# Kernel optimization log

Measured on AMD Instinct MI355X. Metric: run time of the kernel, lower is better.

Reference implementation:

```python
import jax, jax.numpy as jnp
import numpy as np

B_, H_, W_ = 4, 64, 64
D_MODEL, D_INNER, N_STATE, R_RANK, K_ = 96, 192, 16, 6, 4
EPS = 1e-5

def silu(v):
    return v * jax.nn.sigmoid(v)

def setup_inputs() -> dict:
    key = jax.random.key(0)
    ks = jax.random.split(key, 8)
    d, dm = D_INNER, D_MODEL
    A = jnp.tile(jnp.arange(1, N_STATE + 1, dtype=jnp.float32)[None, :], (K_ * d, 1))
    return {
        "x": jax.random.normal(ks[0], (B_, H_, W_, dm), jnp.float32),
        "in_proj_w": jax.random.normal(ks[1], (2 * d, dm), jnp.float32) * 0.02,
        "conv_w": jax.random.normal(ks[2], (d, 1, 3, 3), jnp.float32) * 0.1,
        "conv_b": jnp.zeros((d,), jnp.float32),
        "x_proj_weight": jax.random.normal(ks[3], (K_, R_RANK + 2 * N_STATE, d), jnp.float32) * 0.05,
        "dt_projs_weight": jax.random.normal(ks[4], (K_, d, R_RANK), jnp.float32) * 0.1,
        "dt_projs_bias": jax.random.normal(ks[5], (K_, d), jnp.float32) * 0.1,
        "A_logs": jnp.log(A),
        "Ds": jnp.ones((K_ * d,), jnp.float32),
        "out_norm_w": jnp.ones((d,), jnp.float32),
        "out_norm_b": jnp.zeros((d,), jnp.float32),
        "out_proj_w": jax.random.normal(ks[6], (dm, d), jnp.float32) * 0.02,
    }

def selective_scan(u, dts, As, Bs, Cs, Ds, dt_bias):
    # u, dts: [B,K,D,L]; As: [K,D,N]; Bs, Cs: [B,K,N,L]; Ds, dt_bias: [K,D]
    delta = jax.nn.softplus(dts + dt_bias[None, :, :, None])
    dT = jnp.moveaxis(delta, -1, 0)  # [L,B,K,D]
    uT = jnp.moveaxis(u, -1, 0)      # [L,B,K,D]
    BT = jnp.moveaxis(Bs, -1, 0)     # [L,B,K,N]
    CT = jnp.moveaxis(Cs, -1, 0)     # [L,B,K,N]
    h0 = jnp.zeros((u.shape[0], K_, D_INNER, N_STATE), jnp.float32)

    def step(h, inps):
        dt, ut, bt, ct = inps
        h = jnp.exp(dt[..., None] * As[None]) * h + (dt * ut)[..., None] * bt[:, :, None, :]
        y = jnp.einsum('bkdn,bkn->bkd', h, ct)
        return h, y

    _, ys = jax.lax.scan(step, h0, (dT, uT, BT, CT))
    ys = jnp.moveaxis(ys, 0, -1)  # [B,K,D,L]
    return ys + u * Ds[None, :, :, None]

def reference(x, in_proj_w, conv_w, conv_b, x_proj_weight, dt_projs_weight,
              dt_projs_bias, A_logs, Ds, out_norm_w, out_norm_b, out_proj_w):
    B, H, W, dm = x.shape
    d, N, R, K = D_INNER, N_STATE, R_RANK, K_
    L = H * W
    # in_proj + z gate (SiLU)
    xz = jnp.einsum('bhwc,pc->bhwp', x, in_proj_w)  # [B,H,W,2d]
    xc, z = xz[..., :d], xz[..., d:]
    z = silu(z)
    # depthwise conv (NCHW) + SiLU
    xc = jnp.transpose(xc, (0, 3, 1, 2))  # [B,d,H,W]
    xc = jax.lax.conv_general_dilated(
        xc, conv_w, (1, 1), 'SAME', feature_group_count=d,
        dimension_numbers=('NCHW', 'OIHW', 'NCHW')) + conv_b[None, :, None, None]
    xc = silu(xc)
    # cross-scan: 4 directions
    x0 = xc.reshape(B, d, L)                                   # row-major
    x1 = jnp.transpose(xc, (0, 1, 3, 2)).reshape(B, d, L)       # col-major
    xs = jnp.stack([x0, x1, x0[..., ::-1], x1[..., ::-1]], axis=1)  # [B,K,D,L]
    # projections
    x_dbl = jnp.einsum('bkdl,kcd->bkcl', xs, x_proj_weight)
    dts, Bs, Cs = jnp.split(x_dbl, [R, R + N], axis=2)
    dts = jnp.einsum('bkrl,kdr->bkdl', dts, dt_projs_weight)
    As = -jnp.exp(A_logs).reshape(K, d, N)
    ys = selective_scan(xs, dts, As, Bs, Cs, Ds.reshape(K, d), dt_projs_bias)
    # cross-merge
    y_wh = (ys[:, 1] + ys[:, 3, :, ::-1]).reshape(B, d, W, H)
    y_wh = jnp.transpose(y_wh, (0, 1, 3, 2)).reshape(B, d, L)
    y = ys[:, 0] + ys[:, 2, :, ::-1] + y_wh                     # [B,d,L]
    y = jnp.transpose(y.reshape(B, d, H, W), (0, 2, 3, 1))       # [B,H,W,d]
    # out_norm: LayerNorm over channel dim
    mu = jnp.mean(y, axis=-1, keepdims=True)
    var = jnp.mean((y - mu) ** 2, axis=-1, keepdims=True)
    y = out_norm_w * (y - mu) * jax.lax.rsqrt(var + EPS) + out_norm_b
    # gate + out_proj
    y = y * z
    return jnp.einsum('bhwd,cd->bhwc', y, out_proj_w)
```

## Files before the change

### kernel.cpp

```cpp
#include <hip/hip_runtime.h>
#include <math.h>

#define B_ 4
#define HH 64
#define WW 64
#define LL 4096
#define DM 96
#define DI 192
#define NS 16
#define RR 6
#define KK 4
#define NROW (B_ * KK * DI)
#define XSTR 40

__device__ __forceinline__ int pix_of(int k, int l) {
    switch (k) {
        case 0: return l;
        case 1: { int w = l >> 6, h = l & 63; return (h << 6) + w; }
        case 2: return (LL - 1) - l;
        default: { int ll = (LL - 1) - l; int w = ll >> 6, h = ll & 63; return (h << 6) + w; }
    }
}

__device__ __forceinline__ float silu_f(float v) {
    return v * __fdividef(1.f, 1.f + __expf(-v));
}
__device__ __forceinline__ float softplus_f(float x) {
    return (x > 20.f) ? x : __logf(1.f + __expf(x));
}

template<int MODE>
__global__ __launch_bounds__(256)
void gemm_kernel(const float* __restrict__ A, const float* __restrict__ Bw,
                 float* __restrict__ C0, float* __restrict__ C1,
                 int M, int N, int Kd) {
    __shared__ float As[64][33];
    __shared__ float Bs[64][33];
    int tid = threadIdx.x;
    int tx = tid & 15, ty = tid >> 4;
    int m0 = blockIdx.y * 64, n0 = blockIdx.x * 64;
    float acc[4][4] = {};
    for (int k0 = 0; k0 < Kd; k0 += 32) {
        #pragma unroll
        for (int i = 0; i < 8; ++i) {
            int idx = tid + i * 256;
            int r = idx >> 5, c = idx & 31;
            As[r][c] = A[(size_t)(m0 + r) * Kd + k0 + c];
            int rn = n0 + r;
            Bs[r][c] = (rn < N) ? Bw[(size_t)rn * Kd + k0 + c] : 0.f;
        }
        __syncthreads();
        #pragma unroll
        for (int kk = 0; kk < 32; ++kk) {
            float av[4], bv[4];
            #pragma unroll
            for (int i = 0; i < 4; ++i) av[i] = As[ty * 4 + i][kk];
            #pragma unroll
            for (int j = 0; j < 4; ++j) bv[j] = Bs[tx * 4 + j][kk];
            #pragma unroll
            for (int i = 0; i < 4; ++i)
                #pragma unroll
                for (int j = 0; j < 4; ++j)
                    acc[i][j] += av[i] * bv[j];
        }
        __syncthreads();
    }
    #pragma unroll
    for (int i = 0; i < 4; ++i) {
        int m = m0 + ty * 4 + i;
        #pragma unroll
        for (int j = 0; j < 4; ++j) {
            int n = n0 + tx * 4 + j;
            if (n >= N) continue;
            float v = acc[i][j];
            if (MODE == 0) {
                if (n < DI) C0[(size_t)m * DI + n] = v;
                else        C1[(size_t)m * DI + (n - DI)] = silu_f(v);
            } else {
                C0[(size_t)m * N + n] = v;
            }
        }
    }
}

__global__ __launch_bounds__(192)
void conv_kernel(const float* __restrict__ xc, const float* __restrict__ cw,
                 const float* __restrict__ cb, float* __restrict__ out) {
    int p0 = blockIdx.x * 8;
    int b = blockIdx.y;
    int c = threadIdx.x;
    int h = p0 >> 6, w0 = p0 & 63;
    float kw[9];
    #pragma unroll
    for (int j = 0; j < 9; ++j) kw[j] = cw[c * 9 + j];
    float xv[3][10];
    #pragma unroll
    for (int dh = 0; dh < 3; ++dh) {
        int hh = h + dh - 1;
        bool hv = (hh >= 0 && hh < HH);
        #pragma unroll
        for (int j = 0; j < 10; ++j) {
            int ww = w0 + j - 1;
            bool v = hv && (ww >= 0 && ww < WW);
            xv[dh][j] = v ? xc[((size_t)(b << 12) + (hh << 6) + ww) * DI + c] : 0.f;
        }
    }
    float bias = cb[c];
    #pragma unroll
    for (int w = 0; w < 8; ++w) {
        float acc = bias;
        #pragma unroll
        for (int dh = 0; dh < 3; ++dh)
            #pragma unroll
            for (int dc = 0; dc < 3; ++dc)
                acc += xv[dh][w + dc] * kw[dh * 3 + dc];
        out[((size_t)(b << 12) + p0 + w) * DI + c] = silu_f(acc);
    }
}

__global__ __launch_bounds__(256)
void xdbl_kernel(const float* __restrict__ xconv, const float* __restrict__ xpw,
                 float* __restrict__ xdbl) {
    __shared__ float s_x[128][33];
    __shared__ float s_w[40][33];
    int k = blockIdx.y;
    int b = blockIdx.z;
    int l0 = blockIdx.x * 128;
    int tid = threadIdx.x;
    int tx = tid & 7, ty = tid >> 3;
    float acc[4][5] = {};
    const float* wk = xpw + k * 38 * 192;
    for (int k0 = 0; k0 < 192; k0 += 32) {
        #pragma unroll
        for (int it = 0; it < 16; ++it) {
            int idx = tid + it * 256;
            int r = idx >> 5, c = idx & 31;
            int p = pix_of(k, l0 + r);
            s_x[r][c] = xconv[((size_t)(b << 12) + p) * DI + k0 + c];
        }
        #pragma unroll
        for (int it = 0; it < 5; ++it) {
            int idx = tid + it * 256;
            int r = idx >> 5, c = idx & 31;
            s_w[r][c] = (r < 38) ? wk[r * 192 + k0 + c] : 0.f;
        }
        __syncthreads();
        #pragma unroll
        for (int kk = 0; kk < 32; ++kk) {
            float av[4], bv[5];
            #pragma unroll
            for (int i = 0; i < 4; ++i) av[i] = s_x[ty * 4 + i][kk];
            #pragma unroll
            for (int j = 0; j < 5; ++j) bv[j] = s_w[tx * 5 + j][kk];
            #pragma unroll
            for (int i = 0; i < 4; ++i)
                #pragma unroll
                for (int j = 0; j < 5; ++j)
                    acc[i][j] += av[i] * bv[j];
        }
        __syncthreads();
    }
    size_t base = (size_t)((b * KK + k) << 12);
    #pragma unroll
    for (int i = 0; i < 4; ++i) {
        int l = l0 + ty * 4 + i;
        #pragma unroll
        for (int j = 0; j < 5; ++j) {
            int c = tx * 5 + j;
            if (c < 38) xdbl[(base + l) * XSTR + c] = acc[i][j];
        }
    }
}

template<int PHASE, int NCHT>
__global__ __launch_bounds__(192)
void scan_phase(const float* __restrict__ xconv, const float* __restrict__ xdbl,
                const float* __restrict__ dtw, const float* __restrict__ dtb,
                const float* __restrict__ A_logs, const float* __restrict__ Ds,
                float* __restrict__ carryA, float* __restrict__ carryB,
                float* __restrict__ y_acc) {
    constexpr int CHL = LL / NCHT;
    int chunk = blockIdx.x;
    int k = blockIdx.y;
    int b = blockIdx.z;
    int d = threadIdx.x;
    int l0 = chunk * CHL;
    __shared__ float sx[CHL * XSTR];
    const float4* gx = (const float4*)(xdbl + ((size_t)((b * KK + k) << 12) + l0) * XSTR);
    float4* sx4 = (float4*)sx;
    for (int idx = d; idx < CHL * (XSTR / 4); idx += DI) sx4[idx] = gx[idx];

    float wr[RR];
    #pragma unroll
    for (int r = 0; r < RR; ++r) wr[r] = dtw[(k * DI + d) * RR + r];
    float bias = dtb[k * DI + d];
    const float* alog = A_logs + (size_t)(k * DI + d) * NS;
    bool fastA = true;
    #pragma unroll
    for (int n = 0; n < NS; ++n) {
        float an = -__expf(alog[n]);
        fastA = fastA && (fabsf(an + (float)(n + 1)) < 1e-4f * (float)(n + 1));
    }
    float h[NS];
    int row = (b * KK + k) * DI + d;
    if (PHASE == 1) {
        #pragma unroll
        for (int n = 0; n < NS; ++n) h[n] = 0.f;
    } else {
        #pragma unroll
        for (int n = 0; n < NS; ++n) h[n] = carryB[((size_t)chunk * NROW + row) * NS + n];
    }
    float Dk = (PHASE == 3) ? Ds[k * DI + d] : 0.f;
    float sumDelta = 0.f;
    const float* ubase = xconv + (size_t)(b << 12) * DI + d;
    float* ybase = y_acc + (size_t)(b << 12) * DI + d;
    __syncthreads();

    int p_cur = pix_of(k, l0);
    float u_cur = ubase[(size_t)p_cur * DI];
    for (int i = 0; i < CHL; ++i) {
        int p_nxt = 0; float u_nxt = 0.f;
        if (i + 1 < CHL) {
            p_nxt = pix_of(k, l0 + i + 1);
            u_nxt = ubase[(size_t)p_nxt * DI];
        }
        float xrv[XSTR];
        float4* x4 = (float4*)xrv;
        constexpr int NV = (PHASE == 3) ? (XSTR / 4) : 6;
        #pragma unroll
        for (int j = 0; j < NV; ++j) x4[j] = sx4[i * (XSTR / 4) + j];
        float dtraw = bias;
        #pragma unroll
        for (int r = 0; r < RR; ++r) dtraw += xrv[r] * wr[r];
        float delta = softplus_f(dtraw);
        if (PHASE == 1) sumDelta += delta;
        float du = delta * u_cur;
        float y = 0.f;
        if (fastA) {
            float g = __expf(-delta);
            float a = 1.f;
            #pragma unroll
            for (int n = 0; n < NS; ++n) {
                a *= g;
                h[n] = a * h[n] + du * xrv[6 + n];
                if (PHASE == 3) y += h[n] * xrv[22 + n];
            }
        } else {
            #pragma unroll
            for (int n = 0; n < NS; ++n) {
                float a = __expf(delta * (-__expf(alog[n])));
                h[n] = a * h[n] + du * xrv[6 + n];
                if (PHASE == 3) y += h[n] * xrv[22 + n];
            }
        }
        if (PHASE == 3) {
            y += u_cur * Dk;
            atomicAdd(&ybase[(size_t)p_cur * DI], y);
        }
        p_cur = p_nxt;
        u_cur = u_nxt;
    }
    if (PHASE == 1) {
        #pragma unroll
        for (int n = 0; n < NS; ++n) {
            float An = -__expf(alog[n]);
            carryA[((size_t)chunk * NROW + row) * NS + n] = __expf(An * sumDelta);
            carryB[((size_t)chunk * NROW + row) * NS + n] = h[n];
        }
    }
}

template<int NCHT>
__global__ __launch_bounds__(256)
void scan_chunks(const float* __restrict__ carryA, float* __restrict__ carryB) {
    int t = blockIdx.x * 256 + threadIdx.x;
    if (t >= NROW * NS) return;
    float h = 0.f;
    for (int c = 0; c < NCHT; ++c) {
        size_t idx = (size_t)c * (NROW * NS) + t;
        float a = carryA[idx], bb = carryB[idx];
        carryB[idx] = h;
        h = a * h + bb;
    }
}

__global__ __launch_bounds__(256)
void ln_kernel(const float* __restrict__ y_acc, const float* __restrict__ z_silu,
               const float* __restrict__ nw, const float* __restrict__ nb,
               float* __restrict__ out) {
    int pg = blockIdx.x * 4 + (threadIdx.x >> 6);
    int lane = threadIdx.x & 63;
    const float* yr = y_acc + (size_t)pg * DI;
    float v0 = yr[lane], v1 = yr[lane + 64], v2 = yr[lane + 128];
    float s = v0 + v1 + v2;
    float sq = v0 * v0 + v1 * v1 + v2 * v2;
    #pragma unroll
    for (int m = 32; m >= 1; m >>= 1) {
        s  += __shfl_xor(s, m, 64);
        sq += __shfl_xor(sq, m, 64);
    }
    float mu = s * (1.f / 192.f);
    float var = sq * (1.f / 192.f) - mu * mu;
    float rs = rsqrtf(var + 1e-5f);
    const float* zr = z_silu + (size_t)pg * DI;
    float* o = out + (size_t)pg * DI;
    float vv[3] = {v0, v1, v2};
    #pragma unroll
    for (int j = 0; j < 3; ++j) {
        int c = lane + j * 64;
        o[c] = (nw[c] * (vv[j] - mu) * rs + nb[c]) * zr[c];
    }
}

extern "C" void kernel_launch(void* const* d_in, const int* in_sizes, int n_in,
                              void* d_out, int out_size, void* d_ws, size_t ws_size,
                              hipStream_t stream) {
    const float* x        = (const float*)d_in[0];
    const float* in_projw = (const float*)d_in[1];
    const float* conv_w   = (const float*)d_in[2];
    const float* conv_b   = (const float*)d_in[3];
    const float* x_projw  = (const float*)d_in[4];
    const float* dt_w     = (const float*)d_in[5];
    const float* dt_b     = (const float*)d_in[6];
    const float* A_logs   = (const float*)d_in[7];
    const float* Ds       = (const float*)d_in[8];
    const float* nw       = (const float*)d_in[9];
    const float* nb       = (const float*)d_in[10];
    const float* opw      = (const float*)d_in[11];
    float* out = (float*)d_out;
    float* ws = (float*)d_ws;

    const size_t SZ = (size_t)B_ * LL * DI;
    const size_t XD = (size_t)B_ * KK * LL * XSTR;

    const size_t car128 = (size_t)NROW * 128 * NS;
    const size_t need128 = (3 * SZ + XD + 2 * car128) * sizeof(float);
    bool big = (ws_size >= need128);

    float* z_silu = ws;
    float* xc_raw = ws + SZ;
    float* xconv  = ws + 2 * SZ;
    float* xdbl   = ws + 3 * SZ;
    float* carryA = ws + 3 * SZ + XD;
    float* carryB = carryA + (big ? car128 : (size_t)NROW * 64 * NS);
    float* y_acc  = xc_raw;
    float* yln    = xconv;

    gemm_kernel<0><<<dim3(6, 256), 256, 0, stream>>>(x, in_projw, xc_raw, z_silu,
                                                     B_ * LL, 2 * DI, DM);
    conv_kernel<<<dim3(LL / 8, B_), DI, 0, stream>>>(xc_raw, conv_w, conv_b, xconv);
    xdbl_kernel<<<dim3(LL / 128, KK, B_), 256, 0, stream>>>(xconv, x_projw, xdbl);

    if (big) {
        scan_phase<1, 128><<<dim3(128, KK, B_), DI, 0, stream>>>(xconv, xdbl, dt_w, dt_b,
                                                                 A_logs, Ds, carryA, carryB, nullptr);
        scan_chunks<128><<<(NROW * NS + 255) / 256, 256, 0, stream>>>(carryA, carryB);
        hipMemsetAsync(y_acc, 0, SZ * sizeof(float), stream);
        scan_phase<3, 128><<<dim3(128, KK, B_), DI, 0, stream>>>(xconv, xdbl, dt_w, dt_b,
                                                                 A_logs, Ds, carryA, carryB, y_acc);
    } else {
        scan_phase<1, 64><<<dim3(64, KK, B_), DI, 0, stream>>>(xconv, xdbl, dt_w, dt_b,
                                                               A_logs, Ds, carryA, carryB, nullptr);
        scan_chunks<64><<<(NROW * NS + 255) / 256, 256, 0, stream>>>(carryA, carryB);
        hipMemsetAsync(y_acc, 0, SZ * sizeof(float), stream);
        scan_phase<3, 64><<<dim3(64, KK, B_), DI, 0, stream>>>(xconv, xdbl, dt_w, dt_b,
                                                               A_logs, Ds, carryA, carryB, y_acc);
    }
    ln_kernel<<<(B_ * LL) / 4, 256, 0, stream>>>(y_acc, z_silu, nw, nb, yln);
    gemm_kernel<1><<<dim3(2, 256), 256, 0, stream>>>(yln, opw, out, nullptr,
                                                     B_ * LL, DM, DI);
}
```

Measured before the change: 253.7 us.

## Compute x_proj once per pixel for all directions and vectorize GEMM smem reads

```diff
diff --git a/kernel.cpp b/kernel.cpp
--- a/kernel.cpp
+++ b/kernel.cpp
@@ -11,7 +11,8 @@
 #define RR 6
 #define KK 4
 #define NROW (B_ * KK * DI)
-#define XSTR 40
+#define XPS 160
+#define KOFF 40
 
 __device__ __forceinline__ int pix_of(int k, int l) {
     switch (k) {
@@ -34,8 +35,8 @@
 void gemm_kernel(const float* __restrict__ A, const float* __restrict__ Bw,
                  float* __restrict__ C0, float* __restrict__ C1,
                  int M, int N, int Kd) {
-    __shared__ float As[64][33];
-    __shared__ float Bs[64][33];
+    __shared__ float As[32][68];
+    __shared__ float Bs[32][68];
     int tid = threadIdx.x;
     int tx = tid & 15, ty = tid >> 4;
     int m0 = blockIdx.y * 64, n0 = blockIdx.x * 64;
@@ -45,23 +46,22 @@
         for (int i = 0; i < 8; ++i) {
             int idx = tid + i * 256;
             int r = idx >> 5, c = idx & 31;
-            As[r][c] = A[(size_t)(m0 + r) * Kd + k0 + c];
+            As[c][r] = A[(size_t)(m0 + r) * Kd + k0 + c];
             int rn = n0 + r;
-            Bs[r][c] = (rn < N) ? Bw[(size_t)rn * Kd + k0 + c] : 0.f;
+            Bs[c][r] = (rn < N) ? Bw[(size_t)rn * Kd + k0 + c] : 0.f;
         }
         __syncthreads();
         #pragma unroll
         for (int kk = 0; kk < 32; ++kk) {
-            float av[4], bv[4];
-            #pragma unroll
-            for (int i = 0; i < 4; ++i) av[i] = As[ty * 4 + i][kk];
-            #pragma unroll
-            for (int j = 0; j < 4; ++j) bv[j] = Bs[tx * 4 + j][kk];
+            float4 av = *(const float4*)&As[kk][ty * 4];
+            float4 bv = *(const float4*)&Bs[kk][tx * 4];
+            const float* avp = (const float*)&av;
+            const float* bvp = (const float*)&bv;
             #pragma unroll
             for (int i = 0; i < 4; ++i)
                 #pragma unroll
                 for (int j = 0; j < 4; ++j)
-                    acc[i][j] += av[i] * bv[j];
+                    acc[i][j] += avp[i] * bvp[j];
         }
         __syncthreads();
     }
@@ -76,8 +76,13 @@
             if (MODE == 0) {
                 if (n < DI) C0[(size_t)m * DI + n] = v;
                 else        C1[(size_t)m * DI + (n - DI)] = silu_f(v);
+            } else if (MODE == 1) {
+                C0[(size_t)m * N + n] = v;
             } else {
-                C0[(size_t)m * N + n] = v;
+                if (n < 152) {
+                    int kd = n / 38, c = n - kd * 38;
+                    C0[(size_t)m * XPS + kd * KOFF + c] = v;
+                }
             }
         }
     }
@@ -118,77 +123,28 @@
     }
 }
 
-__global__ __launch_bounds__(256)
-void xdbl_kernel(const float* __restrict__ xconv, const float* __restrict__ xpw,
-                 float* __restrict__ xdbl) {
-    __shared__ float s_x[128][33];
-    __shared__ float s_w[40][33];
-    int k = blockIdx.y;
-    int b = blockIdx.z;
-    int l0 = blockIdx.x * 128;
-    int tid = threadIdx.x;
-    int tx = tid & 7, ty = tid >> 3;
-    float acc[4][5] = {};
-    const float* wk = xpw + k * 38 * 192;
-    for (int k0 = 0; k0 < 192; k0 += 32) {
-        #pragma unroll
-        for (int it = 0; it < 16; ++it) {
-            int idx = tid + it * 256;
-            int r = idx >> 5, c = idx & 31;
-            int p = pix_of(k, l0 + r);
-            s_x[r][c] = xconv[((size_t)(b << 12) + p) * DI + k0 + c];
-        }
-        #pragma unroll
-        for (int it = 0; it < 5; ++it) {
-            int idx = tid + it * 256;
-            int r = idx >> 5, c = idx & 31;
-            s_w[r][c] = (r < 38) ? wk[r * 192 + k0 + c] : 0.f;
-        }
-        __syncthreads();
-        #pragma unroll
-        for (int kk = 0; kk < 32; ++kk) {
-            float av[4], bv[5];
-            #pragma unroll
-            for (int i = 0; i < 4; ++i) av[i] = s_x[ty * 4 + i][kk];
-            #pragma unroll
-            for (int j = 0; j < 5; ++j) bv[j] = s_w[tx * 5 + j][kk];
-            #pragma unroll
-            for (int i = 0; i < 4; ++i)
-                #pragma unroll
-                for (int j = 0; j < 5; ++j)
-                    acc[i][j] += av[i] * bv[j];
-        }
-        __syncthreads();
-    }
-    size_t base = (size_t)((b * KK + k) << 12);
-    #pragma unroll
-    for (int i = 0; i < 4; ++i) {
-        int l = l0 + ty * 4 + i;
-        #pragma unroll
-        for (int j = 0; j < 5; ++j) {
-            int c = tx * 5 + j;
-            if (c < 38) xdbl[(base + l) * XSTR + c] = acc[i][j];
-        }
-    }
-}
-
 template<int PHASE, int NCHT>
 __global__ __launch_bounds__(192)
-void scan_phase(const float* __restrict__ xconv, const float* __restrict__ xdbl,
+void scan_phase(const float* __restrict__ xconv, const float* __restrict__ xdblP,
                 const float* __restrict__ dtw, const float* __restrict__ dtb,
                 const float* __restrict__ A_logs, const float* __restrict__ Ds,
                 float* __restrict__ carryA, float* __restrict__ carryB,
                 float* __restrict__ y_acc) {
     constexpr int CHL = LL / NCHT;
+    constexpr int NV4 = (PHASE == 3) ? (KOFF / 4) : 6;
     int chunk = blockIdx.x;
     int k = blockIdx.y;
     int b = blockIdx.z;
     int d = threadIdx.x;
     int l0 = chunk * CHL;
-    __shared__ float sx[CHL * XSTR];
-    const float4* gx = (const float4*)(xdbl + ((size_t)((b * KK + k) << 12) + l0) * XSTR);
+    __shared__ float sx[CHL * NV4 * 4];
     float4* sx4 = (float4*)sx;
-    for (int idx = d; idx < CHL * (XSTR / 4); idx += DI) sx4[idx] = gx[idx];
+    const float* xb = xdblP + ((size_t)(b << 12)) * XPS + k * KOFF;
+    for (int idx = d; idx < CHL * NV4; idx += DI) {
+        int r = idx / NV4, j = idx - r * NV4;
+        int p = pix_of(k, l0 + r);
+        sx4[idx] = *(const float4*)(xb + (size_t)p * XPS + j * 4);
+    }
 
     float wr[RR];
     #pragma unroll
@@ -224,11 +180,10 @@
             p_nxt = pix_of(k, l0 + i + 1);
             u_nxt = ubase[(size_t)p_nxt * DI];
         }
-        float xrv[XSTR];
+        float xrv[NV4 * 4];
         float4* x4 = (float4*)xrv;
-        constexpr int NV = (PHASE == 3) ? (XSTR / 4) : 6;
-        #pragma unroll
-        for (int j = 0; j < NV; ++j) x4[j] = sx4[i * (XSTR / 4) + j];
+        #pragma unroll
+        for (int j = 0; j < NV4; ++j) x4[j] = sx4[i * NV4 + j];
         float dtraw = bias;
         #pragma unroll
         for (int r = 0; r < RR; ++r) dtraw += xrv[r] * wr[r];
@@ -331,7 +286,7 @@
     float* ws = (float*)d_ws;
 
     const size_t SZ = (size_t)B_ * LL * DI;
-    const size_t XD = (size_t)B_ * KK * LL * XSTR;
+    const size_t XD = (size_t)B_ * LL * XPS;
 
     const size_t car128 = (size_t)NROW * 128 * NS;
     const size_t need128 = (3 * SZ + XD + 2 * car128) * sizeof(float);
@@ -340,7 +295,7 @@
     float* z_silu = ws;
     float* xc_raw = ws + SZ;
     float* xconv  = ws + 2 * SZ;
-    float* xdbl   = ws + 3 * SZ;
+    float* xdblP  = ws + 3 * SZ;
     float* carryA = ws + 3 * SZ + XD;
     float* carryB = carryA + (big ? car128 : (size_t)NROW * 64 * NS);
     float* y_acc  = xc_raw;
@@ -349,21 +304,22 @@
     gemm_kernel<0><<<dim3(6, 256), 256, 0, stream>>>(x, in_projw, xc_raw, z_silu,
                                                      B_ * LL, 2 * DI, DM);
     conv_kernel<<<dim3(LL / 8, B_), DI, 0, stream>>>(xc_raw, conv_w, conv_b, xconv);
-    xdbl_kernel<<<dim3(LL / 128, KK, B_), 256, 0, stream>>>(xconv, x_projw, xdbl);
+    gemm_kernel<2><<<dim3(3, 256), 256, 0, stream>>>(xconv, x_projw, xdblP, nullptr,
+                                                     B_ * LL, 152, DI);
 
     if (big) {
-        scan_phase<1, 128><<<dim3(128, KK, B_), DI, 0, stream>>>(xconv, xdbl, dt_w, dt_b,
+        scan_phase<1, 128><<<dim3(128, KK, B_), DI, 0, stream>>>(xconv, xdblP, dt_w, dt_b,
                                                                  A_logs, Ds, carryA, carryB, nullptr);
         scan_chunks<128><<<(NROW * NS + 255) / 256, 256, 0, stream>>>(carryA, carryB);
         hipMemsetAsync(y_acc, 0, SZ * sizeof(float), stream);
-        scan_phase<3, 128><<<dim3(128, KK, B_), DI, 0, stream>>>(xconv, xdbl, dt_w, dt_b,
+        scan_phase<3, 128><<<dim3(128, KK, B_), DI, 0, stream>>>(xconv, xdblP, dt_w, dt_b,
                                                                  A_logs, Ds, carryA, carryB, y_acc);
     } else {
-        scan_phase<1, 64><<<dim3(64, KK, B_), DI, 0, stream>>>(xconv, xdbl, dt_w, dt_b,
+        scan_phase<1, 64><<<dim3(64, KK, B_), DI, 0, stream>>>(xconv, xdblP, dt_w, dt_b,
                                                                A_logs, Ds, carryA, carryB, nullptr);
         scan_chunks<64><<<(NROW * NS + 255) / 256, 256, 0, stream>>>(carryA, carryB);
         hipMemsetAsync(y_acc, 0, SZ * sizeof(float), stream);
-        scan_phase<3, 64><<<dim3(64, KK, B_), DI, 0, stream>>>(xconv, xdbl, dt_w, dt_b,
+        scan_phase<3, 64><<<dim3(64, KK, B_), DI, 0, stream>>>(xconv, xdblP, dt_w, dt_b,
                                                                A_logs, Ds, carryA, carryB, y_acc);
     }
     ln_kernel<<<(B_ * LL) / 4, 256, 0, stream>>>(y_acc, z_silu, nw, nb, yln);
```

After: 219.4 us. 13.5% less time.
